# Kernel optimization log

Measured on AMD Instinct MI355X. Metric: run time of the kernel, lower is better.

The kernel has to match this reference:

```python
import jax, jax.numpy as jnp
import numpy as np

B, N, DIM, H, HD = 8, 1024, 512, 8, 64
INNER = H * HD  # 512
KS = 5


def setup_inputs() -> dict:
    key = jax.random.key(0)
    ks = jax.random.split(key, 9)
    r = lambda k, shape, s=1.0: jax.random.normal(k, shape, dtype=jnp.float32) * s
    return {
        "x_1": r(ks[0], (B, N, DIM)),
        "x_2": r(ks[1], (B, N, DIM)),
        "Wqkv1": r(ks[2], (DIM, 4 * INNER), 0.02),
        "Wqkv2": r(ks[3], (DIM, 4 * INNER), 0.02),
        "Wout1": r(ks[4], (INNER, DIM), 0.02),
        "bout1": jnp.zeros((DIM,), jnp.float32),
        "Wout2": r(ks[5], (INNER, DIM), 0.02),
        "bout2": jnp.zeros((DIM,), jnp.float32),
        "conv_w": r(ks[6], (N, 1, KS), 0.1),   # depthwise Conv1d weight [out=N, in/groups=1, k]
        "conv_b": r(ks[7], (N,), 0.02),
    }


def _split_heads(t):
    # 'b n (h d) -> b h n d'
    b, n, _ = t.shape
    return t.reshape(b, n, H, HD).transpose(0, 2, 1, 3)


def _merge_heads(t):
    # 'b h n d -> b n (h d)'
    b, h, n, d = t.shape
    return t.transpose(0, 2, 1, 3).reshape(b, n, h * d)


def reference(x_1, x_2, Wqkv1, Wqkv2, Wout1, bout1, Wout2, bout2, conv_w, conv_b):
    scale = HD ** (-0.5)
    q1, k1, v1, s1 = map(_split_heads, jnp.split(x_1 @ Wqkv1, 4, axis=-1))
    q2, k2, v2, s2 = map(_split_heads, jnp.split(x_2 @ Wqkv2, 4, axis=-1))

    dots1 = jnp.einsum('bhid,bhjd->bhij', q1, k1) * scale
    dots2 = jnp.einsum('bhid,bhjd->bhij', q2, k2) * scale

    MS = _merge_heads(s1 + s2)  # [b, n, inner_dim]
    # depthwise conv over the feature axis, channels = tokens (n), kernel 5 pad 2
    A = jax.lax.conv_general_dilated(
        MS, conv_w, window_strides=(1,), padding=((KS // 2, KS // 2),),
        dimension_numbers=('NCH', 'OIH', 'NCH'), feature_group_count=N,
    ) + conv_b[None, :, None]
    MSg = jax.nn.sigmoid(A) * MS
    MSh = _split_heads(MSg)
    dots3 = jnp.einsum('bhid,bhjd->bhij', MSh, MSh) * scale

    a1 = jax.nn.softmax(dots1, axis=-1)
    a2 = jax.nn.softmax(dots2, axis=-1)
    a3 = jax.nn.softmax(dots3, axis=-1)

    t1 = jnp.einsum('bhij,bhjd->bhid', a3, v1) + v1
    t1 = jnp.einsum('bhij,bhjd->bhid', a1, t1)
    t2 = jnp.einsum('bhij,bhjd->bhid', a3, v2) + v2
    t2 = jnp.einsum('bhij,bhjd->bhid', a2, t2)

    out1 = _merge_heads(t1) @ Wout1 + bout1
    out2 = _merge_heads(t2) @ Wout2 + bout2
    return (out1, out2)
```

## Files before the change

kernel.cpp:

```cpp
#include <hip/hip_runtime.h>
#include <hip/hip_bf16.h>

#define B_     8
#define N_     1024
#define DIM_   512
#define H_     8
#define HD_    64
#define INNER_ 512
#define QKVC   2048
#define M_     8192

typedef __attribute__((ext_vector_type(8))) short short8;
typedef __attribute__((ext_vector_type(4))) float f32x4;
#define MFMA_BF16 __builtin_amdgcn_mfma_f32_16x16x32_bf16

__device__ __forceinline__ unsigned short f2b(float x) {
    __hip_bfloat16 h = __float2bfloat16(x);
    unsigned short u; __builtin_memcpy(&u, &h, 2); return u;
}
__device__ __forceinline__ unsigned int packsplit(float x) {
    unsigned int hb = f2b(x);
    float fh = __uint_as_float(hb << 16);
    unsigned int lb = f2b(x - fh);
    return (hb << 16) | lb;
}
__device__ __forceinline__ void split8(const float* v, short8& h, short8& l) {
#pragma unroll
    for (int i = 0; i < 8; i++) {
        unsigned int hb = f2b(v[i]);
        float fh = __uint_as_float(hb << 16);
        h[i] = (short)hb; l[i] = (short)f2b(v[i] - fh);
    }
}

__global__ __launch_bounds__(256)
void pack_f32(const float* __restrict__ in, unsigned int* __restrict__ out)
{
    size_t i = ((size_t)blockIdx.x * 256 + threadIdx.x) * 4;
    float4 v = *(const float4*)(in + i);
    uint4 p;
    p.x = packsplit(v.x); p.y = packsplit(v.y);
    p.z = packsplit(v.z); p.w = packsplit(v.w);
    *(uint4*)(out + i) = p;
}

__global__ __launch_bounds__(256)
void pack_wt(const float* __restrict__ W, unsigned int* __restrict__ Wt, int N)
{
    const int n = blockIdx.x * 256 + threadIdx.x;
    const int k0 = blockIdx.y * 4;
    uint4 p;
    p.x = packsplit(W[(size_t)(k0 + 0) * N + n]);
    p.y = packsplit(W[(size_t)(k0 + 1) * N + n]);
    p.z = packsplit(W[(size_t)(k0 + 2) * N + n]);
    p.w = packsplit(W[(size_t)(k0 + 3) * N + n]);
    *(uint4*)&Wt[(size_t)n * 512 + k0] = p;
}

template<bool BIAS, bool PACKK>
__global__ __launch_bounds__(256)
void gemm_mfma(const unsigned int* __restrict__ Ap, const unsigned int* __restrict__ Btp,
               const float* __restrict__ bias, float* __restrict__ Cp,
               int M, int N)
{
    const int K = 512;
    __shared__ __align__(16) unsigned short sA[128 * 64];
    __shared__ __align__(16) unsigned short sB[128 * 64];

    const int t    = threadIdx.x;
    const int lane = t & 63;
    const int w    = t >> 6;
    const int n16  = lane & 15, quad = lane >> 4;
    const int wm   = w >> 1, wn = w & 1;
    const int m0 = blockIdx.y * 128, n0 = blockIdx.x * 128;

    f32x4 acc[4][4];
#pragma unroll
    for (int mt = 0; mt < 4; mt++)
#pragma unroll
        for (int nt = 0; nt < 4; nt++) acc[mt][nt] = (f32x4){0.f, 0.f, 0.f, 0.f};

    const int srow = t >> 1;
    const int kb   = (t & 1) * 16;
    const unsigned int* ag = Ap  + (size_t)(m0 + srow) * K + kb;
    const unsigned int* bg = Btp + (size_t)(n0 + srow) * K + kb;
    const int s7s = srow & 7;
    unsigned short* swA = &sA[srow * 64];
    unsigned short* swB = &sB[srow * 64];

    for (int k0 = 0; k0 < K; k0 += 32) {
        __syncthreads();
#pragma unroll
        for (int i = 0; i < 4; i++) {
            const int kk = kb + i * 4;
            const int ch = kk >> 3;
            const int ho = kk & 4;
            const int c_hi = ((ch    ) ^ s7s) << 3;
            const int c_lo = ((ch + 4) ^ s7s) << 3;
            uint4 va = *(const uint4*)(ag + k0 + i * 4);
            uint4 vb = *(const uint4*)(bg + k0 + i * 4);
            uint2 ha, la, hb, lb;
            ha.x = (va.y & 0xFFFF0000u) | (va.x >> 16);
            ha.y = (va.w & 0xFFFF0000u) | (va.z >> 16);
            la.x = (va.y << 16) | (va.x & 0xFFFFu);
            la.y = (va.w << 16) | (va.z & 0xFFFFu);
            hb.x = (vb.y & 0xFFFF0000u) | (vb.x >> 16);
            hb.y = (vb.w & 0xFFFF0000u) | (vb.z >> 16);
            lb.x = (vb.y << 16) | (vb.x & 0xFFFFu);
            lb.y = (vb.w << 16) | (vb.z & 0xFFFFu);
            *(uint2*)&swA[c_hi + ho] = ha;
            *(uint2*)&swA[c_lo + ho] = la;
            *(uint2*)&swB[c_hi + ho] = hb;
            *(uint2*)&swB[c_lo + ho] = lb;
        }
        __syncthreads();

        short8 Ah[4], Al[4];
#pragma unroll
        for (int mt = 0; mt < 4; mt++) {
            const int row = 64 * wm + 16 * mt + n16;
            const int base = row * 64;
            const int s7 = row & 7;
            Ah[mt] = *(const short8*)&sA[base + (((quad    ) ^ s7) << 3)];
            Al[mt] = *(const short8*)&sA[base + (((quad + 4) ^ s7) << 3)];
        }
#pragma unroll
        for (int nt = 0; nt < 4; nt++) {
            const int row = 64 * wn + 16 * nt + n16;
            const int base = row * 64;
            const int s7 = row & 7;
            short8 Bh = *(const short8*)&sB[base + (((quad    ) ^ s7) << 3)];
            short8 Bl = *(const short8*)&sB[base + (((quad + 4) ^ s7) << 3)];
#pragma unroll
            for (int mt = 0; mt < 4; mt++) {
                acc[mt][nt] = MFMA_BF16(Ah[mt], Bh, acc[mt][nt], 0, 0, 0);
                acc[mt][nt] = MFMA_BF16(Al[mt], Bh, acc[mt][nt], 0, 0, 0);
                acc[mt][nt] = MFMA_BF16(Ah[mt], Bl, acc[mt][nt], 0, 0, 0);
            }
        }
    }

    const bool packout = PACKK && ((n0 >> 9) == 1);
    float bv[4];
#pragma unroll
    for (int nt = 0; nt < 4; nt++)
        bv[nt] = BIAS ? bias[n0 + 64 * wn + 16 * nt + n16] : 0.f;
#pragma unroll
    for (int mt = 0; mt < 4; mt++) {
        const int rbase = m0 + 64 * wm + 16 * mt + 4 * quad;
#pragma unroll
        for (int r = 0; r < 4; r++) {
#pragma unroll
            for (int nt = 0; nt < 4; nt++) {
                const int col = n0 + 64 * wn + 16 * nt + n16;
                const size_t off = (size_t)(rbase + r) * N + col;
                const float v = acc[mt][nt][r] + bv[nt];
                if (packout) ((unsigned int*)Cp)[off] = packsplit(v);
                else         Cp[off] = v;
            }
        }
    }
}

__global__ __launch_bounds__(128)
void convgate_kernel(const float* __restrict__ qkv1, const float* __restrict__ qkv2,
                     const float* __restrict__ convw,
                     const float* __restrict__ convb,
                     float* __restrict__ MSg, unsigned int* __restrict__ MSgp)
{
    __shared__ float ms[INNER_];
    const int blk = blockIdx.x;
    const int n = blk & (N_ - 1);
    const int t = threadIdx.x;

    const float4* q1 = (const float4*)(qkv1 + (size_t)blk * QKVC + 3 * INNER_);
    const float4* q2 = (const float4*)(qkv2 + (size_t)blk * QKVC + 3 * INNER_);
    float4 v1 = q1[t], v2 = q2[t];
    float4 s;
    s.x = v1.x + v2.x; s.y = v1.y + v2.y; s.z = v1.z + v2.z; s.w = v1.w + v2.w;
    *(float4*)&ms[t * 4] = s;
    __syncthreads();

    float w[5];
#pragma unroll
    for (int k = 0; k < 5; k++) w[k] = convw[n * 5 + k];
    const float cb = convb[n];

    float out[4];
#pragma unroll
    for (int ff = 0; ff < 4; ff++) {
        int f = t * 4 + ff;
        float A = cb;
#pragma unroll
        for (int k = 0; k < 5; k++) {
            int idx = f + k - 2;
            if (idx >= 0 && idx < INNER_) A += ms[idx] * w[k];
        }
        float sg = 1.f / (1.f + __expf(-A));
        out[ff] = ms[f] * sg;
    }
    *(float4*)&MSg[(size_t)blk * INNER_ + t * 4] = make_float4(out[0], out[1], out[2], out[3]);
    uint4 p;
    p.x = packsplit(out[0]); p.y = packsplit(out[1]);
    p.z = packsplit(out[2]); p.w = packsplit(out[3]);
    *(uint4*)&MSgp[(size_t)blk * INNER_ + t * 4] = p;
}

template<int NV, bool RESID, bool PACKO, int NPROB>
__global__ __launch_bounds__(512, 2)
void mattn_kernel(const float* __restrict__ Q0, const float* __restrict__ Q1,
                  const unsigned int* __restrict__ K0, const unsigned int* __restrict__ K1,
                  const float* __restrict__ VA0, const float* __restrict__ VA1,
                  const float* __restrict__ VB0, const float* __restrict__ VB1,
                  float* __restrict__ OA0, float* __restrict__ OA1,
                  float* __restrict__ OB0, float* __restrict__ OB1,
                  long long q_sb, long long q_sh, int q_sr,
                  long long k_sb, long long k_sh, int k_sr,
                  long long v_sb, long long v_sh, int v_sr,
                  long long o_sb, long long o_sh, int o_sr)
{
    __shared__ __align__(16) unsigned short sK[64 * 128];
    __shared__ __align__(16) unsigned short sV0[64 * 64];
    __shared__ __align__(16) unsigned short sV1[(NV == 2) ? 64 * 64 : 8];
    __shared__ __align__(16) unsigned short sP[128 * 64];

    const int t    = threadIdx.x;
    const int w    = t >> 6;
    const int lane = t & 63;
    const int n16  = lane & 15;
    const int quad = lane >> 4;

    const int bid = blockIdx.x;
    const int c   = bid & 7;
    const int r1  = bid >> 3;
    const int qt  = r1 & 7;
    const int r2  = r1 >> 3;
    const int g   = r2 & 7;
    const int p   = (NPROB == 2) ? (r2 >> 3) : 0;
    const int bh  = 8 * g + c;
    const int b = bh >> 3, h = bh & 7;
    const int i0 = qt * 128;

    const float* Qb        = (NPROB == 2 && p) ? Q1 : Q0;
    const unsigned int* Kb = (NPROB == 2 && p) ? K1 : K0;
    const float* VAb       = (NPROB == 2 && p) ? VA1 : VA0;
    float* OAb             = (NPROB == 2 && p) ? OA1 : OA0;

    const float* Qg        = Qb  + (size_t)b * q_sb + (size_t)h * q_sh;
    const unsigned int* Kg = Kb  + (size_t)b * k_sb + (size_t)h * k_sh;
    const float* V0g       = VAb + (size_t)b * v_sb + (size_t)h * v_sh;
    const float* V1g = (NV == 2) ? (VB0 + (size_t)b * v_sb + (size_t)h * v_sh) : nullptr;
    float* O0g = OAb + (size_t)b * o_sb + (size_t)h * o_sh;
    float* O1g = (NV == 2) ? (OB0 + (size_t)b * o_sb + (size_t)h * o_sh) : nullptr;

    short8 Qh[2], Ql[2];
#pragma unroll
    for (int s = 0; s < 2; s++) {
        const float* qp = Qg + (size_t)(i0 + 16 * w + n16) * q_sr + 32 * s + 8 * quad;
        float qv[8];
        float4 q0 = *(const float4*)qp;
        float4 q1 = *(const float4*)(qp + 4);
        qv[0]=q0.x; qv[1]=q0.y; qv[2]=q0.z; qv[3]=q0.w;
        qv[4]=q1.x; qv[5]=q1.y; qv[6]=q1.z; qv[7]=q1.w;
        split8(qv, Qh[s], Ql[s]);
    }

    float m_ = -1e30f, l_ = 0.f;
    f32x4 O0a[4], O1a[(NV == 2) ? 4 : 1];
#pragma unroll
    for (int nt = 0; nt < 4; nt++) O0a[nt] = (f32x4){0.f,0.f,0.f,0.f};
    if constexpr (NV == 2) {
#pragma unroll
        for (int nt = 0; nt < 4; nt++) O1a[nt] = (f32x4){0.f,0.f,0.f,0.f};
    }

    const float scale = 0.125f;
    const int prow = 16 * w + n16;
    const int krow = t >> 3, kfc = t & 7;
    const int vc = t & 15, vp = t >> 4;

    for (int j0 = 0; j0 < N_; j0 += 64) {
        __syncthreads();

        {
            const unsigned int* kp = Kg + (size_t)(j0 + krow) * k_sr + 8 * kfc;
            uint4 va = *(const uint4*)kp;
            uint4 vb = *(const uint4*)(kp + 4);
            uint4 hi, lo;
            hi.x = (va.x >> 16) | (va.y & 0xFFFF0000u);
            hi.y = (va.z >> 16) | (va.w & 0xFFFF0000u);
            hi.z = (vb.x >> 16) | (vb.y & 0xFFFF0000u);
            hi.w = (vb.z >> 16) | (vb.w & 0xFFFF0000u);
            lo.x = (va.x & 0xFFFFu) | (va.y << 16);
            lo.y = (va.z & 0xFFFFu) | (va.w << 16);
            lo.z = (vb.x & 0xFFFFu) | (vb.y << 16);
            lo.w = (vb.z & 0xFFFFu) | (vb.w << 16);
            const int r15 = krow & 15;
            *(uint4*)&sK[krow * 128 + (((kfc    ) ^ r15) << 3)] = hi;
            *(uint4*)&sK[krow * 128 + (((kfc + 8) ^ r15) << 3)] = lo;
        }
        {
            const int j = 2 * vp;
            const float* a0 = V0g + (size_t)(j0 + j) * v_sr + 4 * vc;
            float4 va = *(const float4*)a0;
            float4 vb = *(const float4*)(a0 + v_sr);
#pragma unroll
            for (int e = 0; e < 4; e++) {
                float fa = (e==0)?va.x:(e==1)?va.y:(e==2)?va.z:va.w;
                float fb = (e==0)?vb.x:(e==1)?vb.y:(e==2)?vb.z:vb.w;
                unsigned int u = (unsigned int)f2b(fa) | ((unsigned int)f2b(fb) << 16);
                const int d = 4 * vc + e;
                const int phys = (vp >> 2) ^ ((d ^ (d >> 2)) & 7);
                *(unsigned int*)&sV0[d * 64 + (phys << 3) + (j & 7)] = u;
            }
            if constexpr (NV == 2) {
                const float* a1 = V1g + (size_t)(j0 + j) * v_sr + 4 * vc;
                float4 wa = *(const float4*)a1;
                float4 wb = *(const float4*)(a1 + v_sr);
#pragma unroll
                for (int e = 0; e < 4; e++) {
                    float fa = (e==0)?wa.x:(e==1)?wa.y:(e==2)?wa.z:wa.w;
                    float fb = (e==0)?wb.x:(e==1)?wb.y:(e==2)?wb.z:wb.w;
                    unsigned int u = (unsigned int)f2b(fa) | ((unsigned int)f2b(fb) << 16);
                    const int d = 4 * vc + e;
                    const int phys = (vp >> 2) ^ ((d ^ (d >> 2)) & 7);
                    *(unsigned int*)&sV1[d * 64 + (phys << 3) + (j & 7)] = u;
                }
            }
        }
        __syncthreads();

        f32x4 accS[4];
#pragma unroll
        for (int mt = 0; mt < 4; mt++) accS[mt] = (f32x4){0.f,0.f,0.f,0.f};
#pragma unroll
        for (int s = 0; s < 2; s++) {
#pragma unroll
            for (int mt = 0; mt < 4; mt++) {
                const unsigned short* kb2 = &sK[(16 * mt + n16) * 128];
                short8 kh = *(const short8*)&kb2[(((4*s + quad)    ) ^ n16) << 3];
                short8 kl = *(const short8*)&kb2[(((4*s + quad) + 8) ^ n16) << 3];
                accS[mt] = MFMA_BF16(kl, Qh[s], accS[mt], 0, 0, 0);
                accS[mt] = MFMA_BF16(kh, Ql[s], accS[mt], 0, 0, 0);
                accS[mt] = MFMA_BF16(kh, Qh[s], accS[mt], 0, 0, 0);
            }
        }

        float tmax = -1e30f;
#pragma unroll
        for (int mt = 0; mt < 4; mt++)
#pragma unroll
            for (int r = 0; r < 4; r++) tmax = fmaxf(tmax, accS[mt][r]);
        tmax *= scale;
        tmax = fmaxf(tmax, __shfl_xor(tmax, 16));
        tmax = fmaxf(tmax, __shfl_xor(tmax, 32));
        const float mnew = fmaxf(m_, tmax);
        const float alpha = __expf(m_ - mnew);
        m_ = mnew;
        float rsum = 0.f;
#pragma unroll
        for (int mt = 0; mt < 4; mt++) {
            float p0 = __expf(accS[mt][0] * scale - mnew);
            float p1 = __expf(accS[mt][1] * scale - mnew);
            float p2 = __expf(accS[mt][2] * scale - mnew);
            float p3 = __expf(accS[mt][3] * scale - mnew);
            rsum += (p0 + p1) + (p2 + p3);
            uint2 u;
            u.x = (unsigned int)f2b(p0) | ((unsigned int)f2b(p1) << 16);
            u.y = (unsigned int)f2b(p2) | ((unsigned int)f2b(p3) << 16);
            const int phys = (2 * mt + (quad >> 1)) ^ (n16 & 7);
            *(uint2*)&sP[prow * 64 + (phys << 3) + 4 * (quad & 1)] = u;
        }
        rsum += __shfl_xor(rsum, 16);
        rsum += __shfl_xor(rsum, 32);
        l_ = l_ * alpha + rsum;

        float ar[4];
#pragma unroll
        for (int r = 0; r < 4; r++) ar[r] = __shfl(alpha, (quad << 2) + r);
#pragma unroll
        for (int nt = 0; nt < 4; nt++) {
#pragma unroll
            for (int r = 0; r < 4; r++) O0a[nt][r] *= ar[r];
            if constexpr (NV == 2)
#pragma unroll
                for (int r = 0; r < 4; r++) O1a[nt][r] *= ar[r];
        }

#pragma unroll
        for (int s = 0; s < 2; s++) {
            short8 Pf = *(const short8*)&sP[prow * 64 + (((4*s + quad) ^ (n16 & 7)) << 3)];
#pragma unroll
            for (int nt = 0; nt < 4; nt++) {
                const int d = 16 * nt + n16;
                const int phys = (4*s + quad) ^ ((d ^ (d >> 2)) & 7);
                short8 vf = *(const short8*)&sV0[d * 64 + (phys << 3)];
                O0a[nt] = MFMA_BF16(Pf, vf, O0a[nt], 0, 0, 0);
                if constexpr (NV == 2) {
                    short8 vf1 = *(const short8*)&sV1[d * 64 + (phys << 3)];
                    O1a[nt] = MFMA_BF16(Pf, vf1, O1a[nt], 0, 0, 0);
                }
            }
        }
    }

    float linv[4];
#pragma unroll
    for (int r = 0; r < 4; r++) linv[r] = 1.0f / __shfl(l_, (quad << 2) + r);
#pragma unroll
    for (int r = 0; r < 4; r++) {
        const int row = i0 + 16 * w + 4 * quad + r;
#pragma unroll
        for (int nt = 0; nt < 4; nt++) {
            const int col = 16 * nt + n16;
            float v = O0a[nt][r] * linv[r];
            if constexpr (RESID) v += V0g[(size_t)row * v_sr + col];
            if constexpr (PACKO)
                ((unsigned int*)O0g)[(size_t)row * o_sr + col] = packsplit(v);
            else
                O0g[(size_t)row * o_sr + col] = v;
            if constexpr (NV == 2) {
                float v1 = O1a[nt][r] * linv[r];
                if constexpr (RESID) v1 += V1g[(size_t)row * v_sr + col];
                if constexpr (PACKO)
                    ((unsigned int*)O1g)[(size_t)row * o_sr + col] = packsplit(v1);
                else
                    O1g[(size_t)row * o_sr + col] = v1;
            }
        }
    }
}

extern "C" void kernel_launch(void* const* d_in, const int* in_sizes, int n_in,
                              void* d_out, int out_size, void* d_ws, size_t ws_size,
                              hipStream_t stream)
{
    const float* x1    = (const float*)d_in[0];
    const float* x2    = (const float*)d_in[1];
    const float* Wqkv1 = (const float*)d_in[2];
    const float* Wqkv2 = (const float*)d_in[3];
    const float* Wout1 = (const float*)d_in[4];
    const float* bout1 = (const float*)d_in[5];
    const float* Wout2 = (const float*)d_in[6];
    const float* bout2 = (const float*)d_in[7];
    const float* convw = (const float*)d_in[8];
    const float* convb = (const float*)d_in[9];

    const size_t QKV_ELEMS = (size_t)M_ * QKVC;
    const size_t BND_ELEMS = (size_t)M_ * INNER_;
    if (ws_size < (2 * QKV_ELEMS + 5 * BND_ELEMS) * sizeof(float)) return;

    float* ws   = (float*)d_ws;
    float* qkv1 = ws;
    float* qkv2 = qkv1 + QKV_ELEMS;
    float* MSg  = qkv2 + QKV_ELEMS;
    float* u1   = MSg + BND_ELEMS;
    float* u2   = u1 + BND_ELEMS;
    float* t1m  = u2 + BND_ELEMS;
    float* t2m  = t1m + BND_ELEMS;

    unsigned int* x1p   = (unsigned int*)t1m;
    unsigned int* x2p   = (unsigned int*)t2m;
    unsigned int* MSgp  = (unsigned int*)t1m;
    unsigned int* w1pt  = (unsigned int*)u2;
    unsigned int* w2pt  = w1pt + (size_t)QKVC * DIM_;
    unsigned int* wo1pt = (unsigned int*)u1;
    unsigned int* wo2pt = wo1pt + (size_t)DIM_ * DIM_;

    dim3 blk(256);

    pack_f32<<<dim3(M_ * DIM_ / 1024), blk, 0, stream>>>(x1, x1p);
    pack_f32<<<dim3(M_ * DIM_ / 1024), blk, 0, stream>>>(x2, x2p);
    pack_wt<<<dim3(QKVC / 256, DIM_ / 4), blk, 0, stream>>>(Wqkv1, w1pt, QKVC);
    pack_wt<<<dim3(QKVC / 256, DIM_ / 4), blk, 0, stream>>>(Wqkv2, w2pt, QKVC);

    gemm_mfma<false, true><<<dim3(QKVC / 128, M_ / 128), blk, 0, stream>>>(
        x1p, w1pt, nullptr, qkv1, M_, QKVC);
    gemm_mfma<false, true><<<dim3(QKVC / 128, M_ / 128), blk, 0, stream>>>(
        x2p, w2pt, nullptr, qkv2, M_, QKVC);

    convgate_kernel<<<dim3(M_), dim3(128), 0, stream>>>(qkv1, qkv2, convw, convb, MSg, MSgp);

    const long long msg_sb = (long long)N_ * INNER_, msg_sh = HD_;
    const int       msg_sr = INNER_;
    const long long qkv_sb = (long long)N_ * QKVC, qkv_sh = HD_;
    const int       qkv_sr = QKVC;
    const long long u_sb = (long long)H_ * N_ * HD_, u_sh = (long long)N_ * HD_;
    const int       u_sr = HD_;

    mattn_kernel<2, true, false, 1><<<dim3(512), dim3(512), 0, stream>>>(
        MSg, nullptr, MSgp, nullptr,
        qkv1 + 2 * INNER_, nullptr, qkv2 + 2 * INNER_, nullptr,
        u1, nullptr, u2, nullptr,
        msg_sb, msg_sh, msg_sr,
        msg_sb, msg_sh, msg_sr,
        qkv_sb, qkv_sh, qkv_sr,
        u_sb, u_sh, u_sr);

    mattn_kernel<1, false, true, 2><<<dim3(1024), dim3(512), 0, stream>>>(
        qkv1, qkv2,
        (const unsigned int*)qkv1 + INNER_, (const unsigned int*)qkv2 + INNER_,
        u1, u2, nullptr, nullptr,
        t1m, t2m, nullptr, nullptr,
        qkv_sb, qkv_sh, qkv_sr,
        qkv_sb, qkv_sh, qkv_sr,
        u_sb, u_sh, u_sr,
        msg_sb, msg_sh, msg_sr);

    pack_wt<<<dim3(DIM_ / 256, DIM_ / 4), blk, 0, stream>>>(Wout1, wo1pt, DIM_);
    pack_wt<<<dim3(DIM_ / 256, DIM_ / 4), blk, 0, stream>>>(Wout2, wo2pt, DIM_);

    float* out1 = (float*)d_out;
    float* out2 = out1 + (size_t)M_ * DIM_;
    gemm_mfma<true, false><<<dim3(DIM_ / 128, M_ / 128), blk, 0, stream>>>(
        (const unsigned int*)t1m, wo1pt, bout1, out1, M_, DIM_);
    gemm_mfma<true, false><<<dim3(DIM_ / 128, M_ / 128), blk, 0, stream>>>(
        (const unsigned int*)t2m, wo2pt, bout2, out2, M_, DIM_);
}
```

Before: 486.6 us.

## Pre-tile and swizzle QKV GEMM operands and load via global_load_lds

The pack kernels now write the split hi/lo bf16 operands in 128x32 tile order with an XOR swizzle matching the LDS layout. A new GEMM uses global_load_lds to copy each tile straight from global memory into LDS, with no register staging. This aims to cut load instruction overhead and LDS bank conflicts in the two large QKV projection GEMMs. Loads are still not double-buffered, so each k-step waits on its own load between two barriers.

```diff
diff --git a/kernel.cpp b/kernel.cpp
--- a/kernel.cpp
+++ b/kernel.cpp
@@ -32,16 +32,61 @@
         h[i] = (short)hb; l[i] = (short)f2b(v[i] - fh);
     }
 }
+__device__ __forceinline__ void split2x2(float a, float b, unsigned int& h, unsigned int& l) {
+    unsigned int ha = f2b(a), hb = f2b(b);
+    float fa = __uint_as_float(ha << 16), fb = __uint_as_float(hb << 16);
+    h = ha | (hb << 16);
+    l = (unsigned int)f2b(a - fa) | ((unsigned int)f2b(b - fb) << 16);
+}
+
+__device__ __forceinline__ void gll16(const unsigned short* g, unsigned short* l) {
+    __builtin_amdgcn_global_load_lds(
+        (const __attribute__((address_space(1))) void*)g,
+        (__attribute__((address_space(3))) void*)l, 16, 0, 0);
+}
 
 __global__ __launch_bounds__(256)
-void pack_f32(const float* __restrict__ in, unsigned int* __restrict__ out)
+void pack_a_tiled(const float* __restrict__ in, unsigned short* __restrict__ out)
 {
     size_t i = ((size_t)blockIdx.x * 256 + threadIdx.x) * 4;
     float4 v = *(const float4*)(in + i);
-    uint4 p;
-    p.x = packsplit(v.x); p.y = packsplit(v.y);
-    p.z = packsplit(v.z); p.w = packsplit(v.w);
-    *(uint4*)(out + i) = p;
+    const size_t R = i >> 9;
+    const int k  = (int)(i & 511);
+    const int kt = k >> 5, kk = k & 31;
+    const int r  = (int)(R & 127);
+    const size_t rt = R >> 7;
+    unsigned short* tile = out + (((rt << 4) + kt) << 13) + r * 64;
+    unsigned int h01, l01, h23, l23;
+    split2x2(v.x, v.y, h01, l01);
+    split2x2(v.z, v.w, h23, l23);
+    uint2 hv; hv.x = h01; hv.y = h23;
+    uint2 lv; lv.x = l01; lv.y = l23;
+    const int s7 = r & 7;
+    *(uint2*)&tile[(((kk >> 3)     ^ s7) << 3) + (kk & 7)] = hv;
+    *(uint2*)&tile[((((kk >> 3)+4) ^ s7) << 3) + (kk & 7)] = lv;
+}
+
+__global__ __launch_bounds__(256)
+void pack_w_tiled(const float* __restrict__ W, unsigned short* __restrict__ out, int N)
+{
+    const int n  = blockIdx.x * 256 + threadIdx.x;
+    const int k0 = blockIdx.y * 4;
+    float f0 = W[(size_t)(k0 + 0) * N + n];
+    float f1 = W[(size_t)(k0 + 1) * N + n];
+    float f2 = W[(size_t)(k0 + 2) * N + n];
+    float f3 = W[(size_t)(k0 + 3) * N + n];
+    const int r  = n & 127;
+    const size_t rt = n >> 7;
+    const int kt = k0 >> 5, kk = k0 & 31;
+    unsigned short* tile = out + (((rt << 4) + kt) << 13) + r * 64;
+    unsigned int h01, l01, h23, l23;
+    split2x2(f0, f1, h01, l01);
+    split2x2(f2, f3, h23, l23);
+    uint2 hv; hv.x = h01; hv.y = h23;
+    uint2 lv; lv.x = l01; lv.y = l23;
+    const int s7 = r & 7;
+    *(uint2*)&tile[(((kk >> 3)     ^ s7) << 3) + (kk & 7)] = hv;
+    *(uint2*)&tile[((((kk >> 3)+4) ^ s7) << 3) + (kk & 7)] = lv;
 }
 
 __global__ __launch_bounds__(256)
@@ -55,6 +100,90 @@
     p.z = packsplit(W[(size_t)(k0 + 2) * N + n]);
     p.w = packsplit(W[(size_t)(k0 + 3) * N + n]);
     *(uint4*)&Wt[(size_t)n * 512 + k0] = p;
+}
+
+template<bool BIAS, bool PACKK>
+__global__ __launch_bounds__(256)
+void gemm_gll(const unsigned short* __restrict__ At, const unsigned short* __restrict__ Bt,
+              const float* __restrict__ bias, float* __restrict__ Cp,
+              int M, int N)
+{
+    __shared__ __align__(16) unsigned short sA[128 * 64];
+    __shared__ __align__(16) unsigned short sB[128 * 64];
+
+    const int t    = threadIdx.x;
+    const int lane = t & 63;
+    const int w    = t >> 6;
+    const int n16  = lane & 15, quad = lane >> 4;
+    const int wm   = w >> 1, wn = w & 1;
+    const int m0 = blockIdx.y * 128, n0 = blockIdx.x * 128;
+
+    f32x4 acc[4][4];
+#pragma unroll
+    for (int mt = 0; mt < 4; mt++)
+#pragma unroll
+        for (int nt = 0; nt < 4; nt++) acc[mt][nt] = (f32x4){0.f, 0.f, 0.f, 0.f};
+
+    const unsigned short* Ag = At + ((size_t)blockIdx.y << 4) * 8192 + (w * 64 + lane) * 8;
+    const unsigned short* Bg = Bt + ((size_t)blockIdx.x << 4) * 8192 + (w * 64 + lane) * 8;
+    unsigned short* sAw = &sA[w * 512];
+    unsigned short* sBw = &sB[w * 512];
+
+    for (int kt = 0; kt < 16; kt++) {
+        __syncthreads();
+        const size_t ko = (size_t)kt * 8192;
+#pragma unroll
+        for (int i = 0; i < 4; i++) {
+            gll16(Ag + ko + i * 2048, sAw + i * 2048);
+            gll16(Bg + ko + i * 2048, sBw + i * 2048);
+        }
+        __syncthreads();
+
+        short8 Ah[4], Al[4];
+#pragma unroll
+        for (int mt = 0; mt < 4; mt++) {
+            const int row = 64 * wm + 16 * mt + n16;
+            const int base = row * 64;
+            const int s7 = row & 7;
+            Ah[mt] = *(const short8*)&sA[base + (((quad    ) ^ s7) << 3)];
+            Al[mt] = *(const short8*)&sA[base + (((quad + 4) ^ s7) << 3)];
+        }
+#pragma unroll
+        for (int nt = 0; nt < 4; nt++) {
+            const int row = 64 * wn + 16 * nt + n16;
+            const int base = row * 64;
+            const int s7 = row & 7;
+            short8 Bh = *(const short8*)&sB[base + (((quad    ) ^ s7) << 3)];
+            short8 Bl = *(const short8*)&sB[base + (((quad + 4) ^ s7) << 3)];
+#pragma unroll
+            for (int mt = 0; mt < 4; mt++) {
+                acc[mt][nt] = MFMA_BF16(Ah[mt], Bh, acc[mt][nt], 0, 0, 0);
+                acc[mt][nt] = MFMA_BF16(Al[mt], Bh, acc[mt][nt], 0, 0, 0);
+                acc[mt][nt] = MFMA_BF16(Ah[mt], Bl, acc[mt][nt], 0, 0, 0);
+            }
+        }
+    }
+
+    const bool packout = PACKK && ((n0 >> 9) == 1);
+    float bv[4];
+#pragma unroll
+    for (int nt = 0; nt < 4; nt++)
+        bv[nt] = BIAS ? bias[n0 + 64 * wn + 16 * nt + n16] : 0.f;
+#pragma unroll
+    for (int mt = 0; mt < 4; mt++) {
+        const int rbase = m0 + 64 * wm + 16 * mt + 4 * quad;
+#pragma unroll
+        for (int r = 0; r < 4; r++) {
+#pragma unroll
+            for (int nt = 0; nt < 4; nt++) {
+                const int col = n0 + 64 * wn + 16 * nt + n16;
+                const size_t off = (size_t)(rbase + r) * N + col;
+                const float v = acc[mt][nt][r] + bv[nt];
+                if (packout) ((unsigned int*)Cp)[off] = packsplit(v);
+                else         Cp[off] = v;
+            }
+        }
+    }
 }
 
 template<bool BIAS, bool PACKK>
@@ -459,25 +588,25 @@
     float* t1m  = u2 + BND_ELEMS;
     float* t2m  = t1m + BND_ELEMS;
 
-    unsigned int* x1p   = (unsigned int*)t1m;
-    unsigned int* x2p   = (unsigned int*)t2m;
-    unsigned int* MSgp  = (unsigned int*)t1m;
-    unsigned int* w1pt  = (unsigned int*)u2;
-    unsigned int* w2pt  = w1pt + (size_t)QKVC * DIM_;
-    unsigned int* wo1pt = (unsigned int*)u1;
-    unsigned int* wo2pt = wo1pt + (size_t)DIM_ * DIM_;
+    unsigned short* x1t = (unsigned short*)t1m;
+    unsigned short* x2t = (unsigned short*)t2m;
+    unsigned int*   MSgp = (unsigned int*)t1m;
+    unsigned short* w1t = (unsigned short*)u2;
+    unsigned short* w2t = w1t + (size_t)QKVC * DIM_ * 2;
+    unsigned int*   wo1pt = (unsigned int*)u1;
+    unsigned int*   wo2pt = wo1pt + (size_t)DIM_ * DIM_;
 
     dim3 blk(256);
 
-    pack_f32<<<dim3(M_ * DIM_ / 1024), blk, 0, stream>>>(x1, x1p);
-    pack_f32<<<dim3(M_ * DIM_ / 1024), blk, 0, stream>>>(x2, x2p);
-    pack_wt<<<dim3(QKVC / 256, DIM_ / 4), blk, 0, stream>>>(Wqkv1, w1pt, QKVC);
-    pack_wt<<<dim3(QKVC / 256, DIM_ / 4), blk, 0, stream>>>(Wqkv2, w2pt, QKVC);
-
-    gemm_mfma<false, true><<<dim3(QKVC / 128, M_ / 128), blk, 0, stream>>>(
-        x1p, w1pt, nullptr, qkv1, M_, QKVC);
-    gemm_mfma<false, true><<<dim3(QKVC / 128, M_ / 128), blk, 0, stream>>>(
-        x2p, w2pt, nullptr, qkv2, M_, QKVC);
+    pack_a_tiled<<<dim3(M_ * DIM_ / 1024), blk, 0, stream>>>(x1, x1t);
+    pack_a_tiled<<<dim3(M_ * DIM_ / 1024), blk, 0, stream>>>(x2, x2t);
+    pack_w_tiled<<<dim3(QKVC / 256, DIM_ / 4), blk, 0, stream>>>(Wqkv1, w1t, QKVC);
+    pack_w_tiled<<<dim3(QKVC / 256, DIM_ / 4), blk, 0, stream>>>(Wqkv2, w2t, QKVC);
+
+    gemm_gll<false, true><<<dim3(QKVC / 128, M_ / 128), blk, 0, stream>>>(
+        x1t, w1t, nullptr, qkv1, M_, QKVC);
+    gemm_gll<false, true><<<dim3(QKVC / 128, M_ / 128), blk, 0, stream>>>(
+        x2t, w2t, nullptr, qkv2, M_, QKVC);
 
     convgate_kernel<<<dim3(M_), dim3(128), 0, stream>>>(qkv1, qkv2, convw, convb, MSg, MSgp);
 
```

Result: faster. 466.8 us (-4.1%).
